# Optimization experiments

Measured on AMD Instinct MI355X. Metric: run time of the kernel, lower is better.

Reference implementation:

```python
import jax, jax.numpy as jnp
import numpy as np

ROI = 7      # pooled output size
S = 5        # max adaptive samples per bin dim (boxes <= 0.25*120=30px -> ceil(30/7)=5)


def _roi_align(f, boxes):
    """torchvision roi_align, aligned=True, sampling_ratio=-1 (adaptive).
    f: [C,H,W]; boxes: [N,4] normalized xywh. Returns [N,C,ROI,ROI]."""
    C, H, W = f.shape
    fH, fW = jnp.float32(H), jnp.float32(W)
    x1 = boxes[:, 0] * fW - 0.5                 # aligned=True offset
    y1 = boxes[:, 1] * fH - 0.5
    roi_w = boxes[:, 2] * fW
    roi_h = boxes[:, 3] * fH
    bin_w = roi_w / ROI
    bin_h = roi_h / ROI
    gw = jnp.maximum(jnp.ceil(roi_w / ROI), 1.0)   # adaptive grid counts [N]
    gh = jnp.maximum(jnp.ceil(roi_h / ROI), 1.0)
    ph = jnp.arange(ROI, dtype=jnp.float32)
    s = jnp.arange(S, dtype=jnp.float32)
    # sample coords [N, ROI, S]
    ys = y1[:, None, None] + ph[None, :, None] * bin_h[:, None, None] \
         + (s[None, None, :] + 0.5) * bin_h[:, None, None] / gh[:, None, None]
    xs = x1[:, None, None] + ph[None, :, None] * bin_w[:, None, None] \
         + (s[None, None, :] + 0.5) * bin_w[:, None, None] / gw[:, None, None]
    # broadcast to [N, ROI, ROI, S, S]
    y = ys[:, :, None, :, None]
    x = xs[:, None, :, None, :]
    m = ((s[None, None, None, :, None] < gh[:, None, None, None, None]) &
         (s[None, None, None, None, :] < gw[:, None, None, None, None]))
    valid = (y > -1.0) & (y < fH) & (x > -1.0) & (x < fW)
    yc = jnp.clip(y, 0.0, fH - 1.0)
    xc = jnp.clip(x, 0.0, fW - 1.0)
    y0 = jnp.floor(yc).astype(jnp.int32)
    x0 = jnp.floor(xc).astype(jnp.int32)
    yh = jnp.minimum(y0 + 1, H - 1)
    xh = jnp.minimum(x0 + 1, W - 1)
    ly = yc - y0.astype(jnp.float32); hy = 1.0 - ly
    lx = xc - x0.astype(jnp.float32); hx = 1.0 - lx
    scale = (valid & m).astype(f.dtype)
    y = jnp.broadcast_to(y0 * 0, (boxes.shape[0], ROI, ROI, S, S))  # shape anchor (unused)
    w00 = (hy * hx * scale)[None]
    w01 = (hy * lx * scale)[None]
    w10 = (ly * hx * scale)[None]
    w11 = (ly * lx * scale)[None]
    # gathered values: [C, N, ROI, ROI, S, S]
    vals = (w00 * f[:, y0, x0] + w01 * f[:, y0, xh] +
            w10 * f[:, yh, x0] + w11 * f[:, yh, xh])
    count = (gh * gw)[None, :, None, None]
    pooled = vals.sum(axis=(-1, -2)) / count        # [C, N, ROI, ROI]
    return pooled.transpose(1, 0, 2, 3)              # [N, C, ROI, ROI]


def setup_inputs() -> dict:
    key = jax.random.key(0)
    k = jax.random.split(key, 6)
    features = jax.random.normal(k[0], (1, 128, 120, 120), jnp.float32)
    u = jax.random.uniform(k[1], (512, 4), jnp.float32)
    boxes = jnp.stack([u[:, 0] * 0.7, u[:, 1] * 0.7,
                       0.05 + 0.2 * u[:, 2], 0.05 + 0.2 * u[:, 3]], axis=1)
    d_in = 128 * ROI * ROI  # 6272
    W1 = jax.random.normal(k[2], (d_in, 512), jnp.float32) / np.float32(np.sqrt(d_in))
    b1 = jax.random.normal(k[3], (512,), jnp.float32) * 0.01
    W2 = jax.random.normal(k[4], (512, 256), jnp.float32) / np.float32(np.sqrt(512))
    b2 = jax.random.normal(k[5], (256,), jnp.float32) * 0.01
    return {"features": features, "boxes": boxes, "W1": W1, "b1": b1, "W2": W2, "b2": b2}


def reference(features, boxes, W1, b1, W2, b2):
    roi = _roi_align(features[0], boxes)             # [N,128,7,7]
    flat = roi.reshape(roi.shape[0], -1)             # [N,6272] channel-major like torch .view
    h = jax.nn.relu(flat @ W1 + b1)                  # dropout in eval mode = identity
    return h @ W2 + b2                               # [N,256]
```

## Files before the change

kernel.cpp:

```cpp
#include <hip/hip_runtime.h>
#include <hip/hip_bf16.h>
#include <stdint.h>

#define DI __device__ __forceinline__

typedef __attribute__((ext_vector_type(8))) short short8;
typedef __attribute__((ext_vector_type(4))) float f32x4;
typedef __attribute__((ext_vector_type(2))) float f32x2;

constexpr int CH   = 128;
constexpr int FH   = 120;
constexpr int FW   = 120;
constexpr int NBOX = 512;
constexpr int KDIM = 49 * 128;
constexpr int D1   = 512;
constexpr int D2   = 256;
constexpr int SPLITS = 14;
constexpr int KC     = KDIM / SPLITS;

DI float bf2f(uint32_t u16) { union { uint32_t i; float f; } v; v.i = u16 << 16; return v.f; }
DI float bf2f_hi(uint32_t u) { union { uint32_t i; float f; } v; v.i = u & 0xffff0000u; return v.f; }
DI uint16_t f2bf(float f) {
    __hip_bfloat16 h = __float2bfloat16(f);
    union { __hip_bfloat16 h; uint16_t u; } v; v.h = h; return v.u;
}
DI f32x2 sp2(float s) { f32x2 r; r.x = s; r.y = s; return r; }

__global__ __launch_bounds__(256) void k_preft(const float* __restrict__ f,
                                               uint32_t* __restrict__ ft) {
    __shared__ float lds[30 * 129];
    const int v = blockIdx.x, t = threadIdx.x;
    const int y = v >> 2, x0 = (v & 3) * 30;
    for (int e = t; e < 30 * 128; e += 256) {
        int c = e / 30, x = e - c * 30;
        lds[x * 129 + c] = f[c * (FH * FW) + y * FW + x0 + x];
    }
    __syncthreads();
    for (int e = t; e < 30 * 64; e += 256) {
        int x = e >> 6, cp = e & 63;
        float lo = lds[x * 129 + 2 * cp];
        float hi = lds[x * 129 + 2 * cp + 1];
        ft[(y * FW + x0 + x) * 64 + cp] = (uint32_t)f2bf(lo) | ((uint32_t)f2bf(hi) << 16);
    }
}

template<int GW>
DI void roi_body(const uint32_t* __restrict__ ft, uint32_t* __restrict__ A,
                 int wid, int lane, float xbase, float bin_w, float gwf,
                 float ybase, float bin_h, float ghf, int ghi, float cnt) {
#pragma clang fp contract(off)
    int offx0[GW], offxh[GW];
    float hxm[GW], lxm[GW];
#pragma unroll
    for (int j = 0; j < GW; ++j) {
        float xx = xbase + ((float)j + 0.5f) * bin_w / gwf;
        bool vx = (xx > -1.0f) && (xx < 120.0f);
        float xc = fminf(fmaxf(xx, 0.0f), 119.0f);
        int x0 = (int)floorf(xc);
        int xh = min(x0 + 1, 119);
        float lx = xc - (float)x0, hx = 1.0f - lx;
        float mx = vx ? 1.0f : 0.0f;
        hxm[j] = hx * mx; lxm[j] = lx * mx;
        offx0[j] = x0 * 64; offxh[j] = xh * 64;
    }

    f32x2 acc = {0.0f, 0.0f};
    for (int sy = 0; sy < ghi; ++sy) {
        float yy = ybase + ((float)sy + 0.5f) * bin_h / ghf;
        float my = ((yy > -1.0f) && (yy < 120.0f)) ? 1.0f : 0.0f;
        float yc = fminf(fmaxf(yy, 0.0f), 119.0f);
        int y0 = (int)floorf(yc);
        int yh = min(y0 + 1, 119);
        float ly = yc - (float)y0, hy = 1.0f - ly;
        float hym = hy * my, lym = ly * my;
        const uint32_t* r0 = ft + (size_t)(y0 * (FW * 64)) + lane;
        const uint32_t* r1 = ft + (size_t)(yh * (FW * 64)) + lane;
        uint32_t u00[GW], u01[GW], u10[GW], u11[GW];
#pragma unroll
        for (int j = 0; j < GW; ++j) {
            u00[j] = r0[offx0[j]];
            u01[j] = r0[offxh[j]];
            u10[j] = r1[offx0[j]];
            u11[j] = r1[offxh[j]];
        }
#pragma unroll
        for (int j = 0; j < GW; ++j) {
            float w00 = hym * hxm[j], w01 = hym * lxm[j];
            float w10 = lym * hxm[j], w11 = lym * lxm[j];
            f32x2 v00 = {bf2f(u00[j] & 0xffffu), bf2f_hi(u00[j])};
            f32x2 v01 = {bf2f(u01[j] & 0xffffu), bf2f_hi(u01[j])};
            f32x2 v10 = {bf2f(u10[j] & 0xffffu), bf2f_hi(u10[j])};
            f32x2 v11 = {bf2f(u11[j] & 0xffffu), bf2f_hi(u11[j])};
            acc += sp2(w00) * v00 + sp2(w01) * v01 + sp2(w10) * v10 + sp2(w11) * v11;
        }
    }
    const float v0 = acc.x / cnt, v1 = acc.y / cnt;
    A[(size_t)wid * 64 + lane] = (uint32_t)f2bf(v0) | ((uint32_t)f2bf(v1) << 16);
}

__global__ __launch_bounds__(256) void k_roi_w(const uint32_t* __restrict__ ft,
                                               const float* __restrict__ boxes,
                                               const float* __restrict__ W1,
                                               const float* __restrict__ W2,
                                               uint32_t* __restrict__ A,
                                               uint16_t* __restrict__ W1rT,
                                               uint16_t* __restrict__ W2T) {
    __shared__ __align__(16) float lds[128 * 33];
    const int blk = blockIdx.x, t = threadIdx.x;
    if (blk < 6272) {
#pragma clang fp contract(off)
        const int wid  = (blk << 2) + (t >> 6);
        const int lane = t & 63;
        const int box = wid / 49, bin = wid % 49;
        const int ph = bin / 7, pw = bin % 7;

        const float bx = boxes[box * 4 + 0], by = boxes[box * 4 + 1];
        const float bw = boxes[box * 4 + 2], bh = boxes[box * 4 + 3];
        const float x1 = bx * 120.0f - 0.5f;
        const float y1 = by * 120.0f - 0.5f;
        const float roi_w = bw * 120.0f, roi_h = bh * 120.0f;
        const float bin_w = roi_w / 7.0f, bin_h = roi_h / 7.0f;
        const float gwf = fmaxf(ceilf(roi_w / 7.0f), 1.0f);
        const float ghf = fmaxf(ceilf(roi_h / 7.0f), 1.0f);
        const int gwi = (int)gwf, ghi = (int)ghf;
        const float ybase = y1 + (float)ph * bin_h;
        const float xbase = x1 + (float)pw * bin_w;
        const float cnt = ghf * gwf;

        switch (gwi) {
        case 1: roi_body<1>(ft, A, wid, lane, xbase, bin_w, gwf, ybase, bin_h, ghf, ghi, cnt); break;
        case 2: roi_body<2>(ft, A, wid, lane, xbase, bin_w, gwf, ybase, bin_h, ghf, ghi, cnt); break;
        case 3: roi_body<3>(ft, A, wid, lane, xbase, bin_w, gwf, ybase, bin_h, ghf, ghi, cnt); break;
        case 4: roi_body<4>(ft, A, wid, lane, xbase, bin_w, gwf, ybase, bin_h, ghf, ghi, cnt); break;
        default: roi_body<5>(ft, A, wid, lane, xbase, bin_w, gwf, ybase, bin_h, ghf, ghi, cnt); break;
        }
    } else if (blk < 7056) {
        const int vb = blk - 6272;
        const int b = vb % 49, j0 = (vb / 49) * 32;
        for (int e = t; e < 4096; e += 256) {
            int ci = e >> 5, jj = e & 31;
            lds[ci * 33 + jj] = W1[(ci * 49 + b) * D1 + j0 + jj];
        }
        __syncthreads();
        for (int e = t; e < 4096; e += 256) {
            int jj = e >> 7, ci = e & 127;
            W1rT[(size_t)(j0 + jj) * KDIM + b * 128 + ci] = f2bf(lds[ci * 33 + jj]);
        }
    } else {
        const int v2 = blk - 7056;
        const int n0 = (v2 & 7) * 32, k0 = (v2 >> 3) * 128;
        for (int e = t; e < 4096; e += 256) {
            int k = e >> 5, nn = e & 31;
            lds[k * 33 + nn] = W2[(k0 + k) * D2 + n0 + nn];
        }
        __syncthreads();
        for (int e = t; e < 4096; e += 256) {
            int nn = e >> 7, k = e & 127;
            W2T[(n0 + nn) * D1 + k0 + k] = f2bf(lds[k * 33 + nn]);
        }
    }
}

__global__ __launch_bounds__(256) void k_gemm1(const uint16_t* __restrict__ A,
                                               const uint16_t* __restrict__ B,
                                               float* __restrict__ P) {
    __shared__ __align__(16) uint16_t As[128 * 32];
    __shared__ __align__(16) uint16_t Bs[128 * 32];
    const int t = threadIdx.x;
    const int lane = t & 63, w = t >> 6;
    const int wr = w >> 1, wc = w & 1;
    const int m0 = blockIdx.x * 128, n0 = blockIdx.y * 128;
    const int kbase = blockIdx.z * KC;

    f32x4 acc[4][4] = {};
    const int kb = lane >> 4, r16 = lane & 15;

    for (int ks = 0; ks < KC / 32; ++ks) {
        const int kk = kbase + ks * 32;
        __syncthreads();
#pragma unroll
        for (int i = 0; i < 2; ++i) {
            int ch = t + 256 * i;
            int row = ch >> 2, c8 = ch & 3;
            int sw = (row >> 1) & 3;
            const uint16_t* ga = A + (size_t)(m0 + row) * KDIM + kk + c8 * 8;
            *(uint4*)&As[row * 32 + (c8 ^ sw) * 8] = *(const uint4*)ga;
            const uint16_t* gb = B + (size_t)(n0 + row) * KDIM + kk + c8 * 8;
            *(uint4*)&Bs[row * 32 + (c8 ^ sw) * 8] = *(const uint4*)gb;
        }
        __syncthreads();

        short8 af[4], bfr[4];
#pragma unroll
        for (int mi = 0; mi < 4; ++mi) {
            int ar = wr * 64 + mi * 16 + r16;
            af[mi] = *(const short8*)&As[ar * 32 + (kb ^ ((ar >> 1) & 3)) * 8];
        }
#pragma unroll
        for (int ni = 0; ni < 4; ++ni) {
            int br = wc * 64 + ni * 16 + r16;
            bfr[ni] = *(const short8*)&Bs[br * 32 + (kb ^ ((br >> 1) & 3)) * 8];
        }
#pragma unroll
        for (int mi = 0; mi < 4; ++mi)
#pragma unroll
            for (int ni = 0; ni < 4; ++ni)
                acc[mi][ni] = __builtin_amdgcn_mfma_f32_16x16x32_bf16(af[mi], bfr[ni], acc[mi][ni], 0, 0, 0);
    }

    float* outp = P + (size_t)blockIdx.z * (D1 * D1);
#pragma unroll
    for (int mi = 0; mi < 4; ++mi)
#pragma unroll
        for (int ni = 0; ni < 4; ++ni) {
            int row = m0 + wr * 64 + mi * 16 + kb * 4;
            int col = n0 + wc * 64 + ni * 16 + r16;
#pragma unroll
            for (int r = 0; r < 4; ++r)
                outp[(size_t)(row + r) * D1 + col] = acc[mi][ni][r];
        }
}

__global__ __launch_bounds__(256) void k_reduce1(const float* __restrict__ P,
                                                 const float* __restrict__ b1,
                                                 uint16_t* __restrict__ Hm) {
    const int e4 = blockIdx.x * 256 + threadIdx.x;
    const f32x4* P4 = (const f32x4*)P;
    f32x4 s = {};
#pragma unroll
    for (int i = 0; i < SPLITS; ++i) s += P4[(size_t)i * (D1 * D1 / 4) + e4];
    const int c4 = (e4 & 127) * 4;
    uint16_t h[4];
#pragma unroll
    for (int j = 0; j < 4; ++j) h[j] = f2bf(fmaxf(s[j] + b1[c4 + j], 0.0f));
    uint2 pk;
    pk.x = (uint32_t)h[0] | ((uint32_t)h[1] << 16);
    pk.y = (uint32_t)h[2] | ((uint32_t)h[3] << 16);
    *(uint2*)&Hm[(size_t)e4 * 4] = pk;
}

__global__ __launch_bounds__(256) void k_gemm2(const uint16_t* __restrict__ Hm,
                                               const uint16_t* __restrict__ W2T,
                                               const float* __restrict__ b2,
                                               float* __restrict__ out) {
    const int wid  = blockIdx.x * 4 + (threadIdx.x >> 6);
    const int lane = threadIdx.x & 63;
    const int mt = wid >> 4, nt = wid & 15;
    const int m0 = mt * 16, n0 = nt * 16;
    const int g = lane >> 4, i = lane & 15;
    f32x4 acc = {};
#pragma unroll
    for (int kk = 0; kk < D1 / 32; ++kk) {
        short8 a = *(const short8*)&Hm[(m0 + i) * D1 + kk * 32 + g * 8];
        short8 b = *(const short8*)&W2T[(n0 + i) * D1 + kk * 32 + g * 8];
        acc = __builtin_amdgcn_mfma_f32_16x16x32_bf16(a, b, acc, 0, 0, 0);
    }
    const float bias = b2[n0 + i];
#pragma unroll
    for (int r = 0; r < 4; ++r)
        out[(size_t)(m0 + g * 4 + r) * D2 + n0 + i] = acc[r] + bias;
}

extern "C" void kernel_launch(void* const* d_in, const int* in_sizes, int n_in,
                              void* d_out, int out_size, void* d_ws, size_t ws_size,
                              hipStream_t stream) {
    const float* f     = (const float*)d_in[0];
    const float* boxes = (const float*)d_in[1];
    const float* W1    = (const float*)d_in[2];
    const float* b1    = (const float*)d_in[3];
    const float* W2    = (const float*)d_in[4];
    const float* b2    = (const float*)d_in[5];
    float* out = (float*)d_out;

    char* p = (char*)d_ws;
    uint32_t* ft   = (uint32_t*)p; p += (size_t)FH * FW * (CH / 2) * 4;
    uint16_t* W1rT = (uint16_t*)p; p += (size_t)D1 * KDIM * 2;
    uint16_t* W2T  = (uint16_t*)p; p += (size_t)D2 * D1 * 2;
    uint16_t* Ar   = (uint16_t*)p; p += (size_t)NBOX * KDIM * 2;
    float*    Pp   = (float*)p;    p += (size_t)SPLITS * D1 * D1 * 4;
    uint16_t* Hm   = (uint16_t*)p; p += (size_t)D1 * D1 * 2;

    k_preft<<<480, 256, 0, stream>>>(f, ft);
    k_roi_w<<<7088, 256, 0, stream>>>(ft, boxes, W1, W2, (uint32_t*)Ar, W1rT, W2T);
    k_gemm1<<<dim3(4, 4, SPLITS), 256, 0, stream>>>(Ar, W1rT, Pp);
    k_reduce1<<<D1 * D1 / 4 / 256, 256, 0, stream>>>(Pp, b1, Hm);
    k_gemm2<<<(D1 / 16) * (D2 / 16) / 4, 256, 0, stream>>>(Hm, W2T, b2, out);
}
```

Baseline: 64.68 us.

## Fuse split-K reduction into GEMM1 via last-block atomic counter; specialize ROI on GH

The split-K partial reduction with bias and ReLU moves into the GEMM1 kernel. A per-tile atomic counter, reset in the preprocessing kernel, lets the last-arriving split block sum the partials, which removes one kernel launch. The ROI sampling body is also templated on both grid dimensions, so the y loop is fully unrolled and all loads for small grids can be issued together for more memory-level parallelism. In exchange it adds threadfence and atomic overhead, a serialized reduction tail in one block per tile, and 25 template instantiations that grow code size and register pressure.

```diff
diff --git a/kernel.cpp b/kernel.cpp
--- a/kernel.cpp
+++ b/kernel.cpp
@@ -27,9 +27,11 @@
 DI f32x2 sp2(float s) { f32x2 r; r.x = s; r.y = s; return r; }
 
 __global__ __launch_bounds__(256) void k_preft(const float* __restrict__ f,
-                                               uint32_t* __restrict__ ft) {
+                                               uint32_t* __restrict__ ft,
+                                               uint32_t* __restrict__ tilecnt) {
     __shared__ float lds[30 * 129];
     const int v = blockIdx.x, t = threadIdx.x;
+    if (v == 0 && t < 16) tilecnt[t] = 0;
     const int y = v >> 2, x0 = (v & 3) * 30;
     for (int e = t; e < 30 * 128; e += 256) {
         int c = e / 30, x = e - c * 30;
@@ -44,10 +46,10 @@
     }
 }
 
-template<int GW>
+template<int GH, int GW>
 DI void roi_body(const uint32_t* __restrict__ ft, uint32_t* __restrict__ A,
                  int wid, int lane, float xbase, float bin_w, float gwf,
-                 float ybase, float bin_h, float ghf, int ghi, float cnt) {
+                 float ybase, float bin_h, float ghf, float cnt) {
 #pragma clang fp contract(off)
     int offx0[GW], offxh[GW];
     float hxm[GW], lxm[GW];
@@ -63,35 +65,70 @@
         hxm[j] = hx * mx; lxm[j] = lx * mx;
         offx0[j] = x0 * 64; offxh[j] = xh * 64;
     }
-
-    f32x2 acc = {0.0f, 0.0f};
-    for (int sy = 0; sy < ghi; ++sy) {
-        float yy = ybase + ((float)sy + 0.5f) * bin_h / ghf;
+    int offy0[GH], offy1[GH];
+    float hym[GH], lym[GH];
+#pragma unroll
+    for (int s = 0; s < GH; ++s) {
+        float yy = ybase + ((float)s + 0.5f) * bin_h / ghf;
         float my = ((yy > -1.0f) && (yy < 120.0f)) ? 1.0f : 0.0f;
         float yc = fminf(fmaxf(yy, 0.0f), 119.0f);
         int y0 = (int)floorf(yc);
         int yh = min(y0 + 1, 119);
         float ly = yc - (float)y0, hy = 1.0f - ly;
-        float hym = hy * my, lym = ly * my;
-        const uint32_t* r0 = ft + (size_t)(y0 * (FW * 64)) + lane;
-        const uint32_t* r1 = ft + (size_t)(yh * (FW * 64)) + lane;
-        uint32_t u00[GW], u01[GW], u10[GW], u11[GW];
-#pragma unroll
-        for (int j = 0; j < GW; ++j) {
-            u00[j] = r0[offx0[j]];
-            u01[j] = r0[offxh[j]];
-            u10[j] = r1[offx0[j]];
-            u11[j] = r1[offxh[j]];
-        }
-#pragma unroll
-        for (int j = 0; j < GW; ++j) {
-            float w00 = hym * hxm[j], w01 = hym * lxm[j];
-            float w10 = lym * hxm[j], w11 = lym * lxm[j];
-            f32x2 v00 = {bf2f(u00[j] & 0xffffu), bf2f_hi(u00[j])};
-            f32x2 v01 = {bf2f(u01[j] & 0xffffu), bf2f_hi(u01[j])};
-            f32x2 v10 = {bf2f(u10[j] & 0xffffu), bf2f_hi(u10[j])};
-            f32x2 v11 = {bf2f(u11[j] & 0xffffu), bf2f_hi(u11[j])};
-            acc += sp2(w00) * v00 + sp2(w01) * v01 + sp2(w10) * v10 + sp2(w11) * v11;
+        hym[s] = hy * my; lym[s] = ly * my;
+        offy0[s] = y0 * (FW * 64); offy1[s] = yh * (FW * 64);
+    }
+
+    f32x2 acc = {0.0f, 0.0f};
+    if constexpr (GH * GW <= 12) {
+        uint32_t u00[GH][GW], u01[GH][GW], u10[GH][GW], u11[GH][GW];
+#pragma unroll
+        for (int s = 0; s < GH; ++s) {
+            const uint32_t* r0 = ft + offy0[s] + lane;
+            const uint32_t* r1 = ft + offy1[s] + lane;
+#pragma unroll
+            for (int j = 0; j < GW; ++j) {
+                u00[s][j] = r0[offx0[j]];
+                u01[s][j] = r0[offxh[j]];
+                u10[s][j] = r1[offx0[j]];
+                u11[s][j] = r1[offxh[j]];
+            }
+        }
+#pragma unroll
+        for (int s = 0; s < GH; ++s)
+#pragma unroll
+            for (int j = 0; j < GW; ++j) {
+                float w00 = hym[s] * hxm[j], w01 = hym[s] * lxm[j];
+                float w10 = lym[s] * hxm[j], w11 = lym[s] * lxm[j];
+                f32x2 v00 = {bf2f(u00[s][j] & 0xffffu), bf2f_hi(u00[s][j])};
+                f32x2 v01 = {bf2f(u01[s][j] & 0xffffu), bf2f_hi(u01[s][j])};
+                f32x2 v10 = {bf2f(u10[s][j] & 0xffffu), bf2f_hi(u10[s][j])};
+                f32x2 v11 = {bf2f(u11[s][j] & 0xffffu), bf2f_hi(u11[s][j])};
+                acc += sp2(w00) * v00 + sp2(w01) * v01 + sp2(w10) * v10 + sp2(w11) * v11;
+            }
+    } else {
+#pragma unroll
+        for (int s = 0; s < GH; ++s) {
+            const uint32_t* r0 = ft + offy0[s] + lane;
+            const uint32_t* r1 = ft + offy1[s] + lane;
+            uint32_t u00[GW], u01[GW], u10[GW], u11[GW];
+#pragma unroll
+            for (int j = 0; j < GW; ++j) {
+                u00[j] = r0[offx0[j]];
+                u01[j] = r0[offxh[j]];
+                u10[j] = r1[offx0[j]];
+                u11[j] = r1[offxh[j]];
+            }
+#pragma unroll
+            for (int j = 0; j < GW; ++j) {
+                float w00 = hym[s] * hxm[j], w01 = hym[s] * lxm[j];
+                float w10 = lym[s] * hxm[j], w11 = lym[s] * lxm[j];
+                f32x2 v00 = {bf2f(u00[j] & 0xffffu), bf2f_hi(u00[j])};
+                f32x2 v01 = {bf2f(u01[j] & 0xffffu), bf2f_hi(u01[j])};
+                f32x2 v10 = {bf2f(u10[j] & 0xffffu), bf2f_hi(u10[j])};
+                f32x2 v11 = {bf2f(u11[j] & 0xffffu), bf2f_hi(u11[j])};
+                acc += sp2(w00) * v00 + sp2(w01) * v01 + sp2(w10) * v10 + sp2(w11) * v11;
+            }
         }
     }
     const float v0 = acc.x / cnt, v1 = acc.y / cnt;
@@ -127,13 +164,20 @@
         const float xbase = x1 + (float)pw * bin_w;
         const float cnt = ghf * gwf;
 
-        switch (gwi) {
-        case 1: roi_body<1>(ft, A, wid, lane, xbase, bin_w, gwf, ybase, bin_h, ghf, ghi, cnt); break;
-        case 2: roi_body<2>(ft, A, wid, lane, xbase, bin_w, gwf, ybase, bin_h, ghf, ghi, cnt); break;
-        case 3: roi_body<3>(ft, A, wid, lane, xbase, bin_w, gwf, ybase, bin_h, ghf, ghi, cnt); break;
-        case 4: roi_body<4>(ft, A, wid, lane, xbase, bin_w, gwf, ybase, bin_h, ghf, ghi, cnt); break;
-        default: roi_body<5>(ft, A, wid, lane, xbase, bin_w, gwf, ybase, bin_h, ghf, ghi, cnt); break;
-        }
+#define RB(GH, GW) roi_body<GH, GW>(ft, A, wid, lane, xbase, bin_w, gwf, ybase, bin_h, ghf, cnt)
+        switch (ghi * 8 + gwi) {
+        case  9: RB(1,1); break; case 10: RB(1,2); break; case 11: RB(1,3); break;
+        case 12: RB(1,4); break; case 13: RB(1,5); break;
+        case 17: RB(2,1); break; case 18: RB(2,2); break; case 19: RB(2,3); break;
+        case 20: RB(2,4); break; case 21: RB(2,5); break;
+        case 25: RB(3,1); break; case 26: RB(3,2); break; case 27: RB(3,3); break;
+        case 28: RB(3,4); break; case 29: RB(3,5); break;
+        case 33: RB(4,1); break; case 34: RB(4,2); break; case 35: RB(4,3); break;
+        case 36: RB(4,4); break; case 37: RB(4,5); break;
+        case 41: RB(5,1); break; case 42: RB(5,2); break; case 43: RB(5,3); break;
+        case 44: RB(5,4); break; default: RB(5,5); break;
+        }
+#undef RB
     } else if (blk < 7056) {
         const int vb = blk - 6272;
         const int b = vb % 49, j0 = (vb / 49) * 32;
@@ -161,11 +205,15 @@
     }
 }
 
-__global__ __launch_bounds__(256) void k_gemm1(const uint16_t* __restrict__ A,
-                                               const uint16_t* __restrict__ B,
-                                               float* __restrict__ P) {
+__global__ __launch_bounds__(256) void k_gemm1r(const uint16_t* __restrict__ A,
+                                                const uint16_t* __restrict__ B,
+                                                float* __restrict__ P,
+                                                const float* __restrict__ b1,
+                                                uint16_t* __restrict__ Hm,
+                                                uint32_t* __restrict__ tilecnt) {
     __shared__ __align__(16) uint16_t As[128 * 32];
     __shared__ __align__(16) uint16_t Bs[128 * 32];
+    __shared__ int lastFlag;
     const int t = threadIdx.x;
     const int lane = t & 63, w = t >> 6;
     const int wr = w >> 1, wc = w & 1;
@@ -219,24 +267,33 @@
             for (int r = 0; r < 4; ++r)
                 outp[(size_t)(row + r) * D1 + col] = acc[mi][ni][r];
         }
-}
-
-__global__ __launch_bounds__(256) void k_reduce1(const float* __restrict__ P,
-                                                 const float* __restrict__ b1,
-                                                 uint16_t* __restrict__ Hm) {
-    const int e4 = blockIdx.x * 256 + threadIdx.x;
+
+    __threadfence();
+    if (t == 0) {
+        uint32_t old = __hip_atomic_fetch_add(&tilecnt[blockIdx.x * 4 + blockIdx.y], 1u,
+                                              __ATOMIC_ACQ_REL, __HIP_MEMORY_SCOPE_AGENT);
+        lastFlag = (old == SPLITS - 1);
+    }
+    __syncthreads();
+    if (!lastFlag) return;
+    __threadfence();
+
     const f32x4* P4 = (const f32x4*)P;
-    f32x4 s = {};
-#pragma unroll
-    for (int i = 0; i < SPLITS; ++i) s += P4[(size_t)i * (D1 * D1 / 4) + e4];
-    const int c4 = (e4 & 127) * 4;
-    uint16_t h[4];
-#pragma unroll
-    for (int j = 0; j < 4; ++j) h[j] = f2bf(fmaxf(s[j] + b1[c4 + j], 0.0f));
-    uint2 pk;
-    pk.x = (uint32_t)h[0] | ((uint32_t)h[1] << 16);
-    pk.y = (uint32_t)h[2] | ((uint32_t)h[3] << 16);
-    *(uint2*)&Hm[(size_t)e4 * 4] = pk;
+    for (int g = t; g < 4096; g += 256) {
+        const int r = g >> 5, c4 = g & 31;
+        const f32x4* src = P4 + (size_t)(m0 + r) * 128 + (n0 >> 2) + c4;
+        f32x4 s = {};
+#pragma unroll
+        for (int i = 0; i < SPLITS; ++i) s += src[(size_t)i * (D1 * D1 / 4)];
+        const int colb = n0 + c4 * 4;
+        uint16_t h[4];
+#pragma unroll
+        for (int j = 0; j < 4; ++j) h[j] = f2bf(fmaxf(s[j] + b1[colb + j], 0.0f));
+        uint2 pk;
+        pk.x = (uint32_t)h[0] | ((uint32_t)h[1] << 16);
+        pk.y = (uint32_t)h[2] | ((uint32_t)h[3] << 16);
+        *(uint2*)&Hm[(size_t)(m0 + r) * D1 + colb] = pk;
+    }
 }
 
 __global__ __launch_bounds__(256) void k_gemm2(const uint16_t* __restrict__ Hm,
@@ -279,10 +336,10 @@
     uint16_t* Ar   = (uint16_t*)p; p += (size_t)NBOX * KDIM * 2;
     float*    Pp   = (float*)p;    p += (size_t)SPLITS * D1 * D1 * 4;
     uint16_t* Hm   = (uint16_t*)p; p += (size_t)D1 * D1 * 2;
-
-    k_preft<<<480, 256, 0, stream>>>(f, ft);
+    uint32_t* tc   = (uint32_t*)p; p += 64;
+
+    k_preft<<<480, 256, 0, stream>>>(f, ft, tc);
     k_roi_w<<<7088, 256, 0, stream>>>(ft, boxes, W1, W2, (uint32_t*)Ar, W1rT, W2T);
-    k_gemm1<<<dim3(4, 4, SPLITS), 256, 0, stream>>>(Ar, W1rT, Pp);
-    k_reduce1<<<D1 * D1 / 4 / 256, 256, 0, stream>>>(Pp, b1, Hm);
+    k_gemm1r<<<dim3(4, 4, SPLITS), 256, 0, stream>>>(Ar, W1rT, Pp, b1, Hm, tc);
     k_gemm2<<<(D1 / 16) * (D2 / 16) / 4, 256, 0, stream>>>(Hm, W2T, b2, out);
 }
```

New measurement: 105.9 us. 1.64x slower.

## Split ROI bilinear corners across half-waves with 8-byte loads and full GH/GW unroll

Applied to the files above, without the earlier changes.

Each wave now assigns its two 32-lane halves to the left and right x-corners, and each lane loads two packed bf16 pairs (4 channels) with one 8-byte load. The partial sums are combined with a cross-half shuffle, and only the first half writes the result. Both the y and x sample counts become template parameters, so the sample loops fully unroll, and all loads are issued up front when the grid is small. The aim is fewer, wider loads and more memory-level parallelism in the gather phase. The cost is 25 template instantiations (code size), higher register pressure, and an extra shuffle.

```diff
diff --git a/kernel.cpp b/kernel.cpp
--- a/kernel.cpp
+++ b/kernel.cpp
@@ -24,7 +24,13 @@
     __hip_bfloat16 h = __float2bfloat16(f);
     union { __hip_bfloat16 h; uint16_t u; } v; v.h = h; return v.u;
 }
-DI f32x2 sp2(float s) { f32x2 r; r.x = s; r.y = s; return r; }
+DI f32x4 sp4(float s) { f32x4 r; r.x = s; r.y = s; r.z = s; r.w = s; return r; }
+DI f32x4 up4(uint2 q) {
+    f32x4 r;
+    r.x = bf2f(q.x & 0xffffu); r.y = bf2f_hi(q.x);
+    r.z = bf2f(q.y & 0xffffu); r.w = bf2f_hi(q.y);
+    return r;
+}
 
 __global__ __launch_bounds__(256) void k_preft(const float* __restrict__ f,
                                                uint32_t* __restrict__ ft) {
@@ -44,13 +50,14 @@
     }
 }
 
-template<int GW>
+template<int GH, int GW>
 DI void roi_body(const uint32_t* __restrict__ ft, uint32_t* __restrict__ A,
                  int wid, int lane, float xbase, float bin_w, float gwf,
-                 float ybase, float bin_h, float ghf, int ghi, float cnt) {
+                 float ybase, float bin_h, float ghf, float cnt) {
 #pragma clang fp contract(off)
-    int offx0[GW], offxh[GW];
-    float hxm[GW], lxm[GW];
+    const int side = lane >> 5, cl = lane & 31;
+    int off[GW];
+    float wx[GW];
 #pragma unroll
     for (int j = 0; j < GW; ++j) {
         float xx = xbase + ((float)j + 0.5f) * bin_w / gwf;
@@ -60,42 +67,68 @@
         int xh = min(x0 + 1, 119);
         float lx = xc - (float)x0, hx = 1.0f - lx;
         float mx = vx ? 1.0f : 0.0f;
-        hxm[j] = hx * mx; lxm[j] = lx * mx;
-        offx0[j] = x0 * 64; offxh[j] = xh * 64;
-    }
-
-    f32x2 acc = {0.0f, 0.0f};
-    for (int sy = 0; sy < ghi; ++sy) {
-        float yy = ybase + ((float)sy + 0.5f) * bin_h / ghf;
+        wx[j]  = (side ? lx : hx) * mx;
+        off[j] = (side ? xh : x0) * 64 + 2 * cl;
+    }
+    int offy0[GH], offy1[GH];
+    float hym[GH], lym[GH];
+#pragma unroll
+    for (int s = 0; s < GH; ++s) {
+        float yy = ybase + ((float)s + 0.5f) * bin_h / ghf;
         float my = ((yy > -1.0f) && (yy < 120.0f)) ? 1.0f : 0.0f;
         float yc = fminf(fmaxf(yy, 0.0f), 119.0f);
         int y0 = (int)floorf(yc);
         int yh = min(y0 + 1, 119);
         float ly = yc - (float)y0, hy = 1.0f - ly;
-        float hym = hy * my, lym = ly * my;
-        const uint32_t* r0 = ft + (size_t)(y0 * (FW * 64)) + lane;
-        const uint32_t* r1 = ft + (size_t)(yh * (FW * 64)) + lane;
-        uint32_t u00[GW], u01[GW], u10[GW], u11[GW];
-#pragma unroll
-        for (int j = 0; j < GW; ++j) {
-            u00[j] = r0[offx0[j]];
-            u01[j] = r0[offxh[j]];
-            u10[j] = r1[offx0[j]];
-            u11[j] = r1[offxh[j]];
-        }
-#pragma unroll
-        for (int j = 0; j < GW; ++j) {
-            float w00 = hym * hxm[j], w01 = hym * lxm[j];
-            float w10 = lym * hxm[j], w11 = lym * lxm[j];
-            f32x2 v00 = {bf2f(u00[j] & 0xffffu), bf2f_hi(u00[j])};
-            f32x2 v01 = {bf2f(u01[j] & 0xffffu), bf2f_hi(u01[j])};
-            f32x2 v10 = {bf2f(u10[j] & 0xffffu), bf2f_hi(u10[j])};
-            f32x2 v11 = {bf2f(u11[j] & 0xffffu), bf2f_hi(u11[j])};
-            acc += sp2(w00) * v00 + sp2(w01) * v01 + sp2(w10) * v10 + sp2(w11) * v11;
-        }
-    }
-    const float v0 = acc.x / cnt, v1 = acc.y / cnt;
-    A[(size_t)wid * 64 + lane] = (uint32_t)f2bf(v0) | ((uint32_t)f2bf(v1) << 16);
+        hym[s] = hy * my; lym[s] = ly * my;
+        offy0[s] = y0 * (FW * 64); offy1[s] = yh * (FW * 64);
+    }
+
+    f32x4 acc = {0.0f, 0.0f, 0.0f, 0.0f};
+    if constexpr (GH * GW <= 12) {
+        uint2 q0[GH][GW], q1[GH][GW];
+#pragma unroll
+        for (int s = 0; s < GH; ++s) {
+            const uint32_t* r0 = ft + offy0[s];
+            const uint32_t* r1 = ft + offy1[s];
+#pragma unroll
+            for (int j = 0; j < GW; ++j) {
+                q0[s][j] = *(const uint2*)(r0 + off[j]);
+                q1[s][j] = *(const uint2*)(r1 + off[j]);
+            }
+        }
+#pragma unroll
+        for (int s = 0; s < GH; ++s)
+#pragma unroll
+            for (int j = 0; j < GW; ++j)
+                acc += sp4(hym[s] * wx[j]) * up4(q0[s][j])
+                     + sp4(lym[s] * wx[j]) * up4(q1[s][j]);
+    } else {
+#pragma unroll
+        for (int s = 0; s < GH; ++s) {
+            const uint32_t* r0 = ft + offy0[s];
+            const uint32_t* r1 = ft + offy1[s];
+            uint2 q0[GW], q1[GW];
+#pragma unroll
+            for (int j = 0; j < GW; ++j) {
+                q0[j] = *(const uint2*)(r0 + off[j]);
+                q1[j] = *(const uint2*)(r1 + off[j]);
+            }
+#pragma unroll
+            for (int j = 0; j < GW; ++j)
+                acc += sp4(hym[s] * wx[j]) * up4(q0[j])
+                     + sp4(lym[s] * wx[j]) * up4(q1[j]);
+        }
+    }
+    f32x4 tot;
+#pragma unroll
+    for (int i = 0; i < 4; ++i) tot[i] = acc[i] + __shfl_xor((float)acc[i], 32);
+    if (side == 0) {
+        uint2 pk;
+        pk.x = (uint32_t)f2bf(tot.x / cnt) | ((uint32_t)f2bf(tot.y / cnt) << 16);
+        pk.y = (uint32_t)f2bf(tot.z / cnt) | ((uint32_t)f2bf(tot.w / cnt) << 16);
+        *(uint2*)(A + (size_t)wid * 64 + 2 * cl) = pk;
+    }
 }
 
 __global__ __launch_bounds__(256) void k_roi_w(const uint32_t* __restrict__ ft,
@@ -127,13 +160,20 @@
         const float xbase = x1 + (float)pw * bin_w;
         const float cnt = ghf * gwf;
 
-        switch (gwi) {
-        case 1: roi_body<1>(ft, A, wid, lane, xbase, bin_w, gwf, ybase, bin_h, ghf, ghi, cnt); break;
-        case 2: roi_body<2>(ft, A, wid, lane, xbase, bin_w, gwf, ybase, bin_h, ghf, ghi, cnt); break;
-        case 3: roi_body<3>(ft, A, wid, lane, xbase, bin_w, gwf, ybase, bin_h, ghf, ghi, cnt); break;
-        case 4: roi_body<4>(ft, A, wid, lane, xbase, bin_w, gwf, ybase, bin_h, ghf, ghi, cnt); break;
-        default: roi_body<5>(ft, A, wid, lane, xbase, bin_w, gwf, ybase, bin_h, ghf, ghi, cnt); break;
-        }
+#define RB(GH, GW) roi_body<GH, GW>(ft, A, wid, lane, xbase, bin_w, gwf, ybase, bin_h, ghf, cnt)
+        switch (ghi * 8 + gwi) {
+        case  9: RB(1,1); break; case 10: RB(1,2); break; case 11: RB(1,3); break;
+        case 12: RB(1,4); break; case 13: RB(1,5); break;
+        case 17: RB(2,1); break; case 18: RB(2,2); break; case 19: RB(2,3); break;
+        case 20: RB(2,4); break; case 21: RB(2,5); break;
+        case 25: RB(3,1); break; case 26: RB(3,2); break; case 27: RB(3,3); break;
+        case 28: RB(3,4); break; case 29: RB(3,5); break;
+        case 33: RB(4,1); break; case 34: RB(4,2); break; case 35: RB(4,3); break;
+        case 36: RB(4,4); break; case 37: RB(4,5); break;
+        case 41: RB(5,1); break; case 42: RB(5,2); break; case 43: RB(5,3); break;
+        case 44: RB(5,4); break; default: RB(5,5); break;
+        }
+#undef RB
     } else if (blk < 7056) {
         const int vb = blk - 6272;
         const int b = vb % 49, j0 = (vb / 49) * 32;
```

After: 63.55 us. No clear change (-1.8%).
